# Performance work log

Measured on AMD Instinct MI355X. Metric: run time of the kernel, lower is better.

The kernel has to match this reference:

```python
import jax, jax.numpy as jnp
import numpy as np

R = 40000      # aug_num_rels
E = 500000     # number of relation-graph triplets
DIN = 64       # rel_emb_dim
DH = 64        # hid_dim_rel
H = 8          # num_head
DHID = DH // H # 8
NBIN = 10
L = 2          # num_layer_rel


def _leaky(x):
    return jax.nn.leaky_relu(x, negative_slope=0.2)


def _rel_layer(emb_rel, head, tail, binidx, pw, pb, abin, avec, aw, ab):
    # emb_rel: [R, DH]; head/tail/binidx: [E]
    concat = jnp.concatenate([emb_rel[head], emb_rel[tail]], axis=-1)  # [E, 2*DH]
    z = _leaky(concat @ pw + pb).reshape(-1, H, DHID)                   # [E, H, DHID]
    # attention logits: per-head dot with attn_vec + leaky(bin bias)
    raw = (z * avec[None]).sum(-1) + _leaky(abin[binidx, :, 0])         # [E, H]
    # segmented softmax over edges grouped by head index
    m = jax.ops.segment_max(raw, head, num_segments=R)                  # [R, H]
    e = jnp.exp(raw - m[head])                                          # [E, H]
    s = jax.ops.segment_sum(e, head, num_segments=R)                    # [R, H]
    beta = e / (s[head] + 1e-16)                                        # [E, H]
    msg = (emb_rel[tail] @ aw + ab).reshape(-1, H, DHID) * beta[..., None]
    out = jax.ops.segment_sum(msg, head, num_segments=R)                # [R, H, DHID]
    return out.reshape(R, DH)


def setup_inputs() -> dict:
    key = jax.random.key(0)
    ks = jax.random.split(key, 12)
    ht = jax.random.randint(ks[0], (E, 2), 0, R)
    b = jax.random.randint(ks[1], (E, 1), 0, NBIN)
    relation_triplets = jnp.concatenate([ht, b], axis=-1).astype(jnp.int64)
    sc = 0.05
    return {
        "relation_triplets": relation_triplets,
        "rel_emb_w": jax.random.normal(ks[2], (R, DIN), jnp.float32) * sc,
        "proj1_w": jax.random.normal(ks[3], (DIN, DH), jnp.float32) * sc,
        "proj1_b": jnp.zeros((DH,), jnp.float32),
        "attn_proj_w": jax.random.normal(ks[4], (L, 2 * DH, DH), jnp.float32) * sc,
        "attn_proj_b": jnp.zeros((L, DH), jnp.float32),
        "attn_bin": jax.random.normal(ks[5], (L, NBIN, H, 1), jnp.float32) * sc,
        "attn_vec": jax.random.normal(ks[6], (L, H, DHID), jnp.float32) * sc,
        "aggr_w": jax.random.normal(ks[7], (L, DH, DH), jnp.float32) * sc,
        "aggr_b": jnp.zeros((L, DH), jnp.float32),
        "res_w": jax.random.normal(ks[8], (L, DH, DH), jnp.float32) * sc,
        "res_b": jnp.zeros((L, DH), jnp.float32),
    }


def reference(relation_triplets, rel_emb_w, proj1_w, proj1_b, attn_proj_w,
              attn_proj_b, attn_bin, attn_vec, aggr_w, aggr_b, res_w, res_b):
    head = relation_triplets[:, 0]
    tail = relation_triplets[:, 1]
    binidx = relation_triplets[:, 2]
    emb_rel = jax.nn.relu(rel_emb_w @ proj1_w + proj1_b)  # [R, DH]
    for l in range(L):
        h = _rel_layer(emb_rel, head, tail, binidx,
                       attn_proj_w[l], attn_proj_b[l], attn_bin[l],
                       attn_vec[l], aggr_w[l], aggr_b[l])
        h = jax.nn.relu(h)
        emb_rel = h + jax.nn.relu(emb_rel @ res_w[l] + res_b[l])
    return emb_rel
```

## Files before the change

### kernel.cpp

```cpp
#include <hip/hip_runtime.h>
#include <hip/hip_bf16.h>

typedef __hip_bfloat16 bf16;

#define R_NUM 40000
#define E_NUM 500000
#define HIST_BLOCKS 1954
#define XFA_BLOCKS 1250

#define N_CNTS 0
#define N_ROWP 160000
#define N_STB 320000
#define N_XMP0 2320384
#define N_HR0 12560384
#define N_XMP1 33040384
#define N_HR1 43280384
#define NEED2 63760384ull

#define W_P1W 0
#define W_P1B 4096
#define W_APW 4160
#define W_APB 20544
#define W_ABIN 20672
#define W_AVEC 20832
#define W_AW 20960
#define W_AB 29152
#define W_RW 29280
#define W_RB 37472
#define W_END 37600
#define WCONV_BLOCKS 147

#define O_FLAG 0
#define O_WBUF 256
#define O_ROWP 150784
#define O_CNTS 310784
#define O_TMP 470784
#define O_PART 634624
#define O_STB 635136
#define O_BIG 2635392

static __device__ __forceinline__ float b2f(bf16 x) { return __bfloat162float(x); }
static __device__ __forceinline__ float ldv(const float* p, size_t i) { return p[i]; }
static __device__ __forceinline__ float ldv(const bf16* p, size_t i) { return __bfloat162float(p[i]); }
static __device__ __forceinline__ void stv(float* p, size_t i, float v) { p[i] = v; }
static __device__ __forceinline__ void stv(bf16* p, size_t i, float v) { p[i] = __float2bfloat16(v); }

static __device__ __forceinline__ unsigned int f2bb(float x) {
  union { float f; unsigned int u; } v;
  v.f = x;
  unsigned int r = v.u + 0x7FFFu + ((v.u >> 16) & 1u);
  return r >> 16;
}
static __device__ __forceinline__ unsigned int packxm(float xt, float mt) {
  return f2bb(xt) | (f2bb(mt) << 16);
}

static __device__ __forceinline__ void load_edge(const unsigned int* __restrict__ w, int e,
                                                 int i64, int& h, int& t, int& b) {
  if (i64) {
    h = (int)w[6 * e + 0];
    t = (int)w[6 * e + 2];
    b = (int)w[6 * e + 4];
  } else {
    h = (int)w[3 * e + 0];
    t = (int)w[3 * e + 1];
    b = (int)w[3 * e + 2];
  }
}


__global__ void k_detect_init(const unsigned int* __restrict__ trip_w,
                              const unsigned short* __restrict__ emb_w, int* __restrict__ flag,
                              int* __restrict__ counts, int* __restrict__ stb) {
  int tid = threadIdx.x;
  if (blockIdx.x == 0) {
    if (tid < 64) {
      int lane = tid;
      unsigned int acc = 0;
      for (int i = lane; i < 1024; i += 64) acc |= trip_w[2 * i + 1];
      int votes = 0;
      for (int i = lane; i < 2048; i += 64) {
        unsigned short u = emb_w[2 * i];
        int ex = (u >> 7) & 0xFF;
        if (ex >= 90 && ex <= 130) votes++;
      }
      for (int off = 1; off < 64; off <<= 1) {
        acc |= __shfl_xor(acc, off);
        votes += __shfl_xor(votes, off);
      }
      if (lane == 0) {
        flag[0] = (acc == 0) ? 1 : 0;
        flag[1] = (votes < 1024) ? 1 : 0;
      }
    }
    return;
  }
  int g = (blockIdx.x - 1) * 256 + tid;
  for (int i = g; i < R_NUM; i += 159 * 256) counts[i] = 0;
  if (blockIdx.x == 1 && tid < 64) stb[E_NUM + tid] = 0;
}


template <typename WT, int N>
static __device__ __forceinline__ void xf4t(const float (*sA)[64], int base, int j, int l,
                                            const WT* __restrict__ apw, const WT* __restrict__ apb,
                                            const WT* __restrict__ aw, const WT* __restrict__ ab,
                                            const WT* __restrict__ rw, const WT* __restrict__ rb,
                                            int r0, unsigned int* __restrict__ XMp,
                                            float2* __restrict__ HR) {
  const WT* pwt = apw + l * 8192;
  const WT* pwb = pwt + 4096;
  const WT* awl = aw + l * 4096;
  const WT* rwl = rw + l * 4096;
  float axt[N] = {};
  float amt[N] = {};
  float axh[N] = {};
  float ars[N] = {};
  for (int i4 = 0; i4 < 64; i4 += 4) {
    float4 ev[N];
#pragma unroll
    for (int n = 0; n < N; n++) ev[n] = *(const float4*)&sA[base + n][i4];
#pragma unroll
    for (int di = 0; di < 4; di++) {
      int i = i4 + di;
      float wt = ldv(pwb, (size_t)i * 64 + j);
      float wm = ldv(awl, (size_t)i * 64 + j);
      float wh = ldv(pwt, (size_t)i * 64 + j);
      float wr = ldv(rwl, (size_t)i * 64 + j);
#pragma unroll
      for (int n = 0; n < N; n++) {
        float e = ((const float*)&ev[n])[di];
        axt[n] = fmaf(e, wt, axt[n]);
        amt[n] = fmaf(e, wm, amt[n]);
        axh[n] = fmaf(e, wh, axh[n]);
        ars[n] = fmaf(e, wr, ars[n]);
      }
    }
  }
  float abj = ldv(ab, (size_t)l * 64 + j);
  float pbj = ldv(apb, (size_t)l * 64 + j);
  float rbj = ldv(rb, (size_t)l * 64 + j);
#pragma unroll
  for (int n = 0; n < N; n++) {
    XMp[(size_t)(r0 + n) * 64 + j] = packxm(axt[n], amt[n] + abj);
    HR[(size_t)(r0 + n) * 64 + j] = make_float2(axh[n] + pbj, fmaxf(ars[n] + rbj, 0.f));
  }
}


template <typename T>
static __device__ __forceinline__ void kA_xform(const T* __restrict__ A, const T* __restrict__ p1w,
                                                const T* __restrict__ p1b,
                                                const T* __restrict__ apw,
                                                const T* __restrict__ apb, const T* __restrict__ aw,
                                                const T* __restrict__ ab, const T* __restrict__ rw,
                                                const T* __restrict__ rb, int u,
                                                unsigned int* __restrict__ XMp0,
                                                float2* __restrict__ HR0, float (*sA)[64]) {
  int tid = threadIdx.x;
  int j = tid & 63;
  int g = tid >> 6;
  int base = g * 8;
  for (int k = tid; k < 2048; k += 256) {
    int rr = k >> 6, cc = k & 63;
    sA[rr][cc] = ldv(A, (size_t)(u * 32 + rr) * 64 + cc);
  }
  __syncthreads();
  float a[8] = {0.f, 0.f, 0.f, 0.f, 0.f, 0.f, 0.f, 0.f};
  for (int i4 = 0; i4 < 64; i4 += 4) {
    float4 ev[8];
#pragma unroll
    for (int n = 0; n < 8; n++) ev[n] = *(const float4*)&sA[base + n][i4];
#pragma unroll
    for (int di = 0; di < 4; di++) {
      float wv = ldv(p1w, (size_t)(i4 + di) * 64 + j);
#pragma unroll
      for (int n = 0; n < 8; n++) a[n] = fmaf(((const float*)&ev[n])[di], wv, a[n]);
    }
  }
  float bj = ldv(p1b, j);
#pragma unroll
  for (int n = 0; n < 8; n++) a[n] = fmaxf(a[n] + bj, 0.f);
  __syncthreads();
#pragma unroll
  for (int n = 0; n < 8; n++) sA[base + n][j] = a[n];
  __syncthreads();
  xf4t<T, 8>((const float(*)[64])sA, base, j, 0, apw, apb, aw, ab, rw, rb, u * 32 + base, XMp0,
             HR0);
}

__global__ void __launch_bounds__(256, 4) kA(const unsigned int* __restrict__ trip_w,
                                             const int* __restrict__ flag,
                                             const void* __restrict__ A, const void* p1w,
                                             const void* p1b, const void* apw, const void* apb,
                                             const void* aw, const void* ab, const void* rw,
                                             const void* rb, int* __restrict__ counts,
                                             unsigned int* __restrict__ XMp0,
                                             float2* __restrict__ HR0) {
  if (blockIdx.x >= XFA_BLOCKS) {
    int e = (blockIdx.x - XFA_BLOCKS) * 256 + threadIdx.x;
    if (e < E_NUM) {
      int h = flag[0] ? (int)trip_w[6 * e] : (int)trip_w[3 * e];
      atomicAdd(&counts[h], 1);
    }
    return;
  }
  __shared__ float sA[32][64];
  int u = blockIdx.x;
  if (flag[1])
    kA_xform<float>((const float*)A, (const float*)p1w, (const float*)p1b, (const float*)apw,
                    (const float*)apb, (const float*)aw, (const float*)ab, (const float*)rw,
                    (const float*)rb, u, XMp0, HR0, sA);
  else
    kA_xform<bf16>((const bf16*)A, (const bf16*)p1w, (const bf16*)p1b, (const bf16*)apw,
                   (const bf16*)apb, (const bf16*)aw, (const bf16*)ab, (const bf16*)rw,
                   (const bf16*)rb, u, XMp0, HR0, sA);
}


__global__ void __launch_bounds__(1024) k_scan1(const int* __restrict__ counts,
                                                int* __restrict__ row_ptr) {
  __shared__ int sp[1024];
  int tid = threadIdx.x;
  int base = tid * 40;
  int local[40];
  int s = 0;
  if (base < R_NUM) {
#pragma unroll
    for (int k = 0; k < 40; k++) {
      int v = counts[base + k];
      local[k] = s;
      s += v;
    }
  }
  sp[tid] = s;
  __syncthreads();
  for (int off = 1; off < 1024; off <<= 1) {
    int t = (tid >= off) ? sp[tid - off] : 0;
    __syncthreads();
    sp[tid] += t;
    __syncthreads();
  }
  int pre = (tid == 0) ? 0 : sp[tid - 1];
  if (base < R_NUM) {
#pragma unroll
    for (int k = 0; k < 40; k++) row_ptr[base + k] = pre + local[k];
  }
}

__global__ void k_scatter(const unsigned int* __restrict__ trip_w, const int* __restrict__ flag,
                          int* __restrict__ row_ptr, int* __restrict__ stb) {
  int e = blockIdx.x * 256 + threadIdx.x;
  if (e >= E_NUM) return;
  int h, t, b;
  load_edge(trip_w, e, flag[0], h, t, b);
  int pos = atomicAdd(&row_ptr[h], 1);
  stb[pos] = (t & 0xFFFF) | (b << 16);
}


template <typename T>
static __device__ __forceinline__ void edge_body(int l, const int* __restrict__ row_ptr,
                                                 const int* __restrict__ stb,
                                                 const unsigned int* __restrict__ XMp,
                                                 const float2* __restrict__ HR,
                                                 const T* __restrict__ abin,
                                                 const T* __restrict__ avec,
                                                 float* __restrict__ out, float* sab) {
  int tid = threadIdx.x;
  int lane = tid & 63;
  int w = tid >> 6;
  int hh = lane >> 3;
  if (tid < 80) {
    float a = ldv(abin, (size_t)l * 80 + tid);
    sab[tid] = (a > 0.f) ? a : 0.2f * a;
  }
  __syncthreads();
  float av = ldv(avec, (size_t)l * 64 + lane);

  int r = blockIdx.x * 4 + w;
  float2 hr = HR[(size_t)r * 64 + lane];
  int beg = (r == 0) ? 0 : row_ptr[r - 1];
  int end = row_ptr[r];
  beg = __builtin_amdgcn_readfirstlane(beg);
  end = __builtin_amdgcn_readfirstlane(end);

  float xh = hr.x;
  float num = 0.f, den = 0.f;
  int t0 = (beg < end) ? (stb[beg] & 0xFFFF) : 0;
  for (int jj = beg; jj < end; jj += 16) {
    int pk[16];
    unsigned int xp[16];
#pragma unroll
    for (int k = 0; k < 16; k++) pk[k] = stb[jj + k];
#pragma unroll
    for (int k = 0; k < 16; k++) {
      int t = (jj + k < end) ? (pk[k] & 0xFFFF) : t0;
      xp[k] = XMp[(size_t)t * 64 + lane];
    }
#pragma unroll
    for (int k = 0; k < 16; k++) {
      float xt = __uint_as_float(xp[k] << 16);
      float mt = __uint_as_float(xp[k] & 0xFFFF0000u);
      float z = xh + xt;
      z = (z > 0.f) ? z : 0.2f * z;
      float v = z * av;
      v += __shfl_xor(v, 1);
      v += __shfl_xor(v, 2);
      v += __shfl_xor(v, 4);
      float e = __expf(v + sab[(pk[k] >> 16) * 8 + hh]);
      e = (jj + k < end) ? e : 0.f;
      den += e;
      num = fmaf(mt, e, num);
    }
  }
  out[(size_t)r * 64 + lane] = fmaxf(num / (den + 1e-16f), 0.f) + hr.y;
}

__global__ void __launch_bounds__(256, 8) kE0(const int* __restrict__ row_ptr,
                                              const int* __restrict__ stb,
                                              const int* __restrict__ flag,
                                              const unsigned int* __restrict__ XMp0,
                                              const float2* __restrict__ HR0, const void* abin,
                                              const void* avec, float* __restrict__ emb) {
  __shared__ float sab[80];
  if (flag[1])
    edge_body<float>(0, row_ptr, stb, XMp0, HR0, (const float*)abin, (const float*)avec, emb, sab);
  else
    edge_body<bf16>(0, row_ptr, stb, XMp0, HR0, (const bf16*)abin, (const bf16*)avec, emb, sab);
}

__global__ void __launch_bounds__(256, 8) kC(const int* __restrict__ row_ptr,
                                             const int* __restrict__ stb,
                                             const int* __restrict__ flag,
                                             const unsigned int* __restrict__ XMp1,
                                             const float2* __restrict__ HR1, const void* abin,
                                             const void* avec, float* __restrict__ out) {
  __shared__ float sab[80];
  if (flag[1])
    edge_body<float>(1, row_ptr, stb, XMp1, HR1, (const float*)abin, (const float*)avec, out, sab);
  else
    edge_body<bf16>(1, row_ptr, stb, XMp1, HR1, (const bf16*)abin, (const bf16*)avec, out, sab);
}


template <typename T>
static __device__ __forceinline__ void kX1_body(const float* __restrict__ emb,
                                                const T* __restrict__ apw,
                                                const T* __restrict__ apb, const T* __restrict__ aw,
                                                const T* __restrict__ ab, const T* __restrict__ rw,
                                                const T* __restrict__ rb, int u,
                                                unsigned int* __restrict__ XMp1,
                                                float2* __restrict__ HR1, float (*sE)[64]) {
  int tid = threadIdx.x;
  int j = tid & 63;
  int g = tid >> 6;
  for (int k = tid; k < 2048; k += 256) {
    int rr = k >> 6, cc = k & 63;
    sE[rr][cc] = emb[(size_t)(u * 32 + rr) * 64 + cc];
  }
  __syncthreads();
  xf4t<T, 8>((const float(*)[64])sE, g * 8, j, 1, apw, apb, aw, ab, rw, rb, u * 32 + g * 8, XMp1,
             HR1);
}

__global__ void __launch_bounds__(256, 4) kX1(const float* __restrict__ emb,
                                              const int* __restrict__ flag, const void* apw,
                                              const void* apb, const void* aw, const void* ab,
                                              const void* rw, const void* rb,
                                              unsigned int* __restrict__ XMp1,
                                              float2* __restrict__ HR1) {
  __shared__ float sE[32][64];
  int u = blockIdx.x;
  if (flag[1])
    kX1_body<float>(emb, (const float*)apw, (const float*)apb, (const float*)aw, (const float*)ab,
                    (const float*)rw, (const float*)rb, u, XMp1, HR1, sE);
  else
    kX1_body<bf16>(emb, (const bf16*)apw, (const bf16*)apb, (const bf16*)aw, (const bf16*)ab,
                   (const bf16*)rw, (const bf16*)rb, u, XMp1, HR1, sE);
}


__global__ void k_hist_wconv(const unsigned int* __restrict__ trip_w, const int* __restrict__ flag,
                             int* __restrict__ counts, const void* p1w, const void* p1b,
                             const void* apw, const void* apb, const void* abin, const void* avec,
                             const void* aw, const void* ab, const void* rw, const void* rb,
                             float* __restrict__ wbuf) {
  if (blockIdx.x < WCONV_BLOCKS) {
    int i = blockIdx.x * 256 + threadIdx.x;
    if (i >= W_END) return;
    const void* src;
    int off;
    if (i < W_P1B) { src = p1w; off = i - W_P1W; }
    else if (i < W_APW) { src = p1b; off = i - W_P1B; }
    else if (i < W_APB) { src = apw; off = i - W_APW; }
    else if (i < W_ABIN) { src = apb; off = i - W_APB; }
    else if (i < W_AVEC) { src = abin; off = i - W_ABIN; }
    else if (i < W_AW) { src = avec; off = i - W_AVEC; }
    else if (i < W_AB) { src = aw; off = i - W_AW; }
    else if (i < W_RW) { src = ab; off = i - W_AB; }
    else if (i < W_RB) { src = rw; off = i - W_RW; }
    else { src = rb; off = i - W_RB; }
    wbuf[i] = flag[1] ? ((const float*)src)[off] : b2f(((const bf16*)src)[off]);
    return;
  }
  int e = (blockIdx.x - WCONV_BLOCKS) * 256 + threadIdx.x;
  if (e >= E_NUM) return;
  int h, t, b;
  load_edge(trip_w, e, flag[0], h, t, b);
  atomicAdd(&counts[h], 1);
}

__global__ void k_emb0(const void* __restrict__ A, const int* __restrict__ flag,
                       const float* __restrict__ wbuf, float* __restrict__ emb) {
  int j = threadIdx.x & 63;
  int g = threadIdx.x >> 6;
  int r0 = blockIdx.x * 16 + g * 4;
  int f32 = flag[1];
  __shared__ float sA[16][64];
  for (int k = threadIdx.x; k < 1024; k += 256) {
    int rr = k >> 6, cc = k & 63;
    size_t idx = (size_t)(blockIdx.x * 16 + rr) * 64 + cc;
    sA[rr][cc] = f32 ? ((const float*)A)[idx] : b2f(((const bf16*)A)[idx]);
  }
  __syncthreads();
  const float* W = wbuf + W_P1W;
  float a[4] = {0.f, 0.f, 0.f, 0.f};
  int base = g * 4;
  for (int i = 0; i < 64; i++) {
    float w = W[i * 64 + j];
#pragma unroll
    for (int n = 0; n < 4; n++) a[n] = fmaf(sA[base + n][i], w, a[n]);
  }
  float bj = wbuf[W_P1B + j];
#pragma unroll
  for (int n = 0; n < 4; n++)
    emb[(size_t)(r0 + n) * 64 + j] = fmaxf(a[n] + bj, 0.f);
}

static __device__ __forceinline__ float dotcol(const float* __restrict__ Wm, float val, int lane) {
  float acc = 0.f;
  for (int i = 0; i < 64; i++) acc = fmaf(__shfl(val, i), Wm[i * 64 + lane], acc);
  return acc;
}

template <typename TIN, typename TOUT>
__global__ void k_edge_d(const int* __restrict__ row_ptr, const int* __restrict__ stb,
                         const float* __restrict__ wbuf, int l, const TIN* __restrict__ emb_in,
                         TOUT* __restrict__ emb_out) {
  __shared__ float sab[80];
  int tid = threadIdx.x;
  int lane = tid & 63;
  int w = tid >> 6;
  int r = blockIdx.x * 4 + w;
  int hh = lane >> 3;
  if (tid < 80) {
    float a = wbuf[W_ABIN + l * 80 + tid];
    sab[tid] = (a > 0.f) ? a : 0.2f * a;
  }
  __syncthreads();
  const float* pwt = wbuf + W_APW + l * 8192;
  const float* pwb = pwt + 4096;
  const float* aw = wbuf + W_AW + l * 4096;
  const float* rw = wbuf + W_RW + l * 4096;

  float ev = ldv(emb_in, (size_t)r * 64 + lane);
  float xh = wbuf[W_APB + l * 64 + lane];
  float res = wbuf[W_RB + l * 64 + lane];
  for (int i = 0; i < 64; i++) {
    float e = __shfl(ev, i);
    xh = fmaf(e, pwt[i * 64 + lane], xh);
    res = fmaf(e, rw[i * 64 + lane], res);
  }
  res = fmaxf(res, 0.f);
  float av = wbuf[W_AVEC + l * 64 + lane];
  float abl = wbuf[W_AB + l * 64 + lane];

  int beg = (r == 0) ? 0 : row_ptr[r - 1];
  int end = row_ptr[r];
  float num = 0.f, den = 0.f;
  for (int j = beg; j < end; j++) {
    int p = stb[j];
    int t = p & 0xFFFF;
    float tv = ldv(emb_in, (size_t)t * 64 + lane);
    float z = xh + dotcol(pwb, tv, lane);
    z = (z > 0.f) ? z : 0.2f * z;
    float v = z * av;
    v += __shfl_xor(v, 1);
    v += __shfl_xor(v, 2);
    v += __shfl_xor(v, 4);
    float e = __expf(v + sab[(p >> 16) * 8 + hh]);
    den += e;
    float mt = dotcol(aw, tv, lane) + abl;
    num = fmaf(mt, e, num);
  }
  stv(emb_out, (size_t)r * 64 + lane, fmaxf(num / (den + 1e-16f), 0.f) + res);
}


extern "C" void kernel_launch(void* const* d_in, const int* in_sizes, int n_in,
                              void* d_out, int out_size, void* d_ws, size_t ws_size,
                              hipStream_t stream) {
  const unsigned int* trip_w = (const unsigned int*)d_in[0];
  const void* rel_emb = d_in[1];
  float* emb = (float*)d_out;
  char* ws = (char*)d_ws;

  if (ws_size >= NEED2) {
    int* counts = (int*)(ws + N_CNTS);
    int* row_ptr = (int*)(ws + N_ROWP);
    int* stb = (int*)(ws + N_STB);
    unsigned int* XMp0 = (unsigned int*)(ws + N_XMP0);
    float2* HR0 = (float2*)(ws + N_HR0);
    unsigned int* XMp1 = (unsigned int*)(ws + N_XMP1);
    float2* HR1 = (float2*)(ws + N_HR1);
    int* flag = (int*)(ws + N_STB + (E_NUM + 64) * 4);

    k_detect_init<<<160, 256, 0, stream>>>(trip_w, (const unsigned short*)rel_emb, flag, counts,
                                           stb);
    kA<<<XFA_BLOCKS + HIST_BLOCKS, 256, 0, stream>>>(trip_w, flag, rel_emb, d_in[2], d_in[3],
                                                     d_in[4], d_in[5], d_in[8], d_in[9], d_in[10],
                                                     d_in[11], counts, XMp0, HR0);
    k_scan1<<<1, 1024, 0, stream>>>(counts, row_ptr);
    k_scatter<<<HIST_BLOCKS, 256, 0, stream>>>(trip_w, flag, row_ptr, stb);
    kE0<<<R_NUM / 4, 256, 0, stream>>>(row_ptr, stb, flag, XMp0, HR0, d_in[6], d_in[7], emb);
    kX1<<<XFA_BLOCKS, 256, 0, stream>>>(emb, flag, d_in[4], d_in[5], d_in[8], d_in[9], d_in[10],
                                        d_in[11], XMp1, HR1);
    kC<<<R_NUM / 4, 256, 0, stream>>>(row_ptr, stb, flag, XMp1, HR1, d_in[6], d_in[7], emb);
    return;
  }

  {
    int* flag = (int*)(ws + O_FLAG);
    float* wbuf = (float*)(ws + O_WBUF);
    int* row_ptr = (int*)(ws + O_ROWP);
    int* counts = (int*)(ws + O_CNTS);
    int* stb = (int*)(ws + O_STB);
    char* big = ws + O_BIG;

    k_detect_init<<<160, 256, 0, stream>>>(trip_w, (const unsigned short*)rel_emb, flag, counts,
                                           stb);
    k_hist_wconv<<<WCONV_BLOCKS + HIST_BLOCKS, 256, 0, stream>>>(
        trip_w, flag, counts, d_in[2], d_in[3], d_in[4], d_in[5], d_in[6], d_in[7], d_in[8],
        d_in[9], d_in[10], d_in[11], wbuf);
    k_scan1<<<1, 1024, 0, stream>>>(counts, row_ptr);
    k_scatter<<<HIST_BLOCKS, 256, 0, stream>>>(trip_w, flag, row_ptr, stb);
    k_emb0<<<R_NUM / 16, 256, 0, stream>>>(rel_emb, flag, wbuf, emb);
    bf16* embB = (bf16*)big;
    k_edge_d<float, bf16><<<R_NUM / 4, 256, 0, stream>>>(row_ptr, stb, wbuf, 0, emb, embB);
    k_edge_d<bf16, float><<<R_NUM / 4, 256, 0, stream>>>(row_ptr, stb, wbuf, 1, embB, emb);
  }
}
```

Measured before the change: 258.8 us.

## Record histogram ranks to drop scatter atomics, prefetch weights, grid-stride transforms

The histogram pass now stores each edge's atomicAdd return value as a rank. The scatter then computes its position as row_ptr[h]+rank[e] with no second atomic, and row_ptr becomes an exclusive scan with an extra end entry. The transform kernels also software-prefetch the next four weight rows into registers and run as a fixed grid of 1024 blocks looping over 1250 tiles. This removes contended atomics in the scatter at the cost of an extra 2MB rank buffer, and the prefetching adds register pressure.

Result: slower. 364.5 us (+40.9%).

```diff
diff --git a/kernel.cpp b/kernel.cpp
--- a/kernel.cpp
+++ b/kernel.cpp
@@ -6,16 +6,19 @@
 #define R_NUM 40000
 #define E_NUM 500000
 #define HIST_BLOCKS 1954
-#define XFA_BLOCKS 1250
+#define XF_TILES 1250
+#define XF_GRID 1024
 
 #define N_CNTS 0
 #define N_ROWP 160000
-#define N_STB 320000
-#define N_XMP0 2320384
-#define N_HR0 12560384
-#define N_XMP1 33040384
-#define N_HR1 43280384
-#define NEED2 63760384ull
+#define N_RANK 320256
+#define N_STB 2320384
+#define N_FLAG 4320640
+#define N_XMP0 4320896
+#define N_HR0 14560896
+#define N_XMP1 35040896
+#define N_HR1 45280896
+#define NEED2 65760896ull
 
 #define W_P1W 0
 #define W_P1B 4096
@@ -34,12 +37,12 @@
 #define O_WBUF 256
 #define O_ROWP 150784
 #define O_CNTS 310784
-#define O_TMP 470784
-#define O_PART 634624
 #define O_STB 635136
 #define O_BIG 2635392
 
 static __device__ __forceinline__ float b2f(bf16 x) { return __bfloat162float(x); }
+static __device__ __forceinline__ float cvt(float x) { return x; }
+static __device__ __forceinline__ float cvt(bf16 x) { return __bfloat162float(x); }
 static __device__ __forceinline__ float ldv(const float* p, size_t i) { return p[i]; }
 static __device__ __forceinline__ float ldv(const bf16* p, size_t i) { return __bfloat162float(p[i]); }
 static __device__ __forceinline__ void stv(float* p, size_t i, float v) { p[i] = v; }
@@ -116,17 +119,35 @@
   float amt[N] = {};
   float axh[N] = {};
   float ars[N] = {};
+  WT cw[16];
+#pragma unroll
+  for (int di = 0; di < 4; di++) {
+    size_t o = (size_t)di * 64 + j;
+    cw[di * 4 + 0] = pwb[o];
+    cw[di * 4 + 1] = awl[o];
+    cw[di * 4 + 2] = pwt[o];
+    cw[di * 4 + 3] = rwl[o];
+  }
   for (int i4 = 0; i4 < 64; i4 += 4) {
+    WT nw[16];
+    int i4n = (i4 + 4 < 64) ? i4 + 4 : i4;
+#pragma unroll
+    for (int di = 0; di < 4; di++) {
+      size_t o = (size_t)(i4n + di) * 64 + j;
+      nw[di * 4 + 0] = pwb[o];
+      nw[di * 4 + 1] = awl[o];
+      nw[di * 4 + 2] = pwt[o];
+      nw[di * 4 + 3] = rwl[o];
+    }
     float4 ev[N];
 #pragma unroll
     for (int n = 0; n < N; n++) ev[n] = *(const float4*)&sA[base + n][i4];
 #pragma unroll
     for (int di = 0; di < 4; di++) {
-      int i = i4 + di;
-      float wt = ldv(pwb, (size_t)i * 64 + j);
-      float wm = ldv(awl, (size_t)i * 64 + j);
-      float wh = ldv(pwt, (size_t)i * 64 + j);
-      float wr = ldv(rwl, (size_t)i * 64 + j);
+      float wt = cvt(cw[di * 4 + 0]);
+      float wm = cvt(cw[di * 4 + 1]);
+      float wh = cvt(cw[di * 4 + 2]);
+      float wr = cvt(cw[di * 4 + 3]);
 #pragma unroll
       for (int n = 0; n < N; n++) {
         float e = ((const float*)&ev[n])[di];
@@ -136,6 +157,8 @@
         ars[n] = fmaf(e, wr, ars[n]);
       }
     }
+#pragma unroll
+    for (int k = 0; k < 16; k++) cw[k] = nw[k];
   }
   float abj = ldv(ab, (size_t)l * 64 + j);
   float pbj = ldv(apb, (size_t)l * 64 + j);
@@ -167,16 +190,25 @@
   }
   __syncthreads();
   float a[8] = {0.f, 0.f, 0.f, 0.f, 0.f, 0.f, 0.f, 0.f};
+  T pw[4];
+#pragma unroll
+  for (int di = 0; di < 4; di++) pw[di] = p1w[(size_t)di * 64 + j];
   for (int i4 = 0; i4 < 64; i4 += 4) {
+    T npw[4];
+    int i4n = (i4 + 4 < 64) ? i4 + 4 : i4;
+#pragma unroll
+    for (int di = 0; di < 4; di++) npw[di] = p1w[(size_t)(i4n + di) * 64 + j];
     float4 ev[8];
 #pragma unroll
     for (int n = 0; n < 8; n++) ev[n] = *(const float4*)&sA[base + n][i4];
 #pragma unroll
     for (int di = 0; di < 4; di++) {
-      float wv = ldv(p1w, (size_t)(i4 + di) * 64 + j);
+      float wv = cvt(pw[di]);
 #pragma unroll
       for (int n = 0; n < 8; n++) a[n] = fmaf(((const float*)&ev[n])[di], wv, a[n]);
     }
+#pragma unroll
+    for (int di = 0; di < 4; di++) pw[di] = npw[di];
   }
   float bj = ldv(p1b, j);
 #pragma unroll
@@ -195,26 +227,30 @@
                                              const void* p1b, const void* apw, const void* apb,
                                              const void* aw, const void* ab, const void* rw,
                                              const void* rb, int* __restrict__ counts,
+                                             int* __restrict__ rank,
                                              unsigned int* __restrict__ XMp0,
                                              float2* __restrict__ HR0) {
-  if (blockIdx.x >= XFA_BLOCKS) {
-    int e = (blockIdx.x - XFA_BLOCKS) * 256 + threadIdx.x;
+  if (blockIdx.x >= XF_GRID) {
+    int e = (blockIdx.x - XF_GRID) * 256 + threadIdx.x;
     if (e < E_NUM) {
       int h = flag[0] ? (int)trip_w[6 * e] : (int)trip_w[3 * e];
-      atomicAdd(&counts[h], 1);
+      rank[e] = atomicAdd(&counts[h], 1);
     }
     return;
   }
   __shared__ float sA[32][64];
-  int u = blockIdx.x;
-  if (flag[1])
-    kA_xform<float>((const float*)A, (const float*)p1w, (const float*)p1b, (const float*)apw,
-                    (const float*)apb, (const float*)aw, (const float*)ab, (const float*)rw,
-                    (const float*)rb, u, XMp0, HR0, sA);
-  else
-    kA_xform<bf16>((const bf16*)A, (const bf16*)p1w, (const bf16*)p1b, (const bf16*)apw,
-                   (const bf16*)apb, (const bf16*)aw, (const bf16*)ab, (const bf16*)rw,
-                   (const bf16*)rb, u, XMp0, HR0, sA);
+  int f32 = flag[1];
+  for (int u = blockIdx.x; u < XF_TILES; u += XF_GRID) {
+    if (f32)
+      kA_xform<float>((const float*)A, (const float*)p1w, (const float*)p1b, (const float*)apw,
+                      (const float*)apb, (const float*)aw, (const float*)ab, (const float*)rw,
+                      (const float*)rb, u, XMp0, HR0, sA);
+    else
+      kA_xform<bf16>((const bf16*)A, (const bf16*)p1w, (const bf16*)p1b, (const bf16*)apw,
+                     (const bf16*)apb, (const bf16*)aw, (const bf16*)ab, (const bf16*)rw,
+                     (const bf16*)rb, u, XMp0, HR0, sA);
+    __syncthreads();
+  }
 }
 
 
@@ -246,15 +282,17 @@
 #pragma unroll
     for (int k = 0; k < 40; k++) row_ptr[base + k] = pre + local[k];
   }
-}
-
-__global__ void k_scatter(const unsigned int* __restrict__ trip_w, const int* __restrict__ flag,
-                          int* __restrict__ row_ptr, int* __restrict__ stb) {
+  if (tid == 1023) row_ptr[R_NUM] = sp[1023];
+}
+
+__global__ void k_scatter2(const unsigned int* __restrict__ trip_w, const int* __restrict__ flag,
+                           const int* __restrict__ row_ptr, const int* __restrict__ rank,
+                           int* __restrict__ stb) {
   int e = blockIdx.x * 256 + threadIdx.x;
   if (e >= E_NUM) return;
   int h, t, b;
   load_edge(trip_w, e, flag[0], h, t, b);
-  int pos = atomicAdd(&row_ptr[h], 1);
+  int pos = row_ptr[h] + rank[e];
   stb[pos] = (t & 0xFFFF) | (b << 16);
 }
 
@@ -280,8 +318,8 @@
 
   int r = blockIdx.x * 4 + w;
   float2 hr = HR[(size_t)r * 64 + lane];
-  int beg = (r == 0) ? 0 : row_ptr[r - 1];
-  int end = row_ptr[r];
+  int beg = row_ptr[r];
+  int end = row_ptr[r + 1];
   beg = __builtin_amdgcn_readfirstlane(beg);
   end = __builtin_amdgcn_readfirstlane(end);
 
@@ -371,13 +409,16 @@
                                               unsigned int* __restrict__ XMp1,
                                               float2* __restrict__ HR1) {
   __shared__ float sE[32][64];
-  int u = blockIdx.x;
-  if (flag[1])
-    kX1_body<float>(emb, (const float*)apw, (const float*)apb, (const float*)aw, (const float*)ab,
-                    (const float*)rw, (const float*)rb, u, XMp1, HR1, sE);
-  else
-    kX1_body<bf16>(emb, (const bf16*)apw, (const bf16*)apb, (const bf16*)aw, (const bf16*)ab,
-                   (const bf16*)rw, (const bf16*)rb, u, XMp1, HR1, sE);
+  int f32 = flag[1];
+  for (int u = blockIdx.x; u < XF_TILES; u += XF_GRID) {
+    if (f32)
+      kX1_body<float>(emb, (const float*)apw, (const float*)apb, (const float*)aw,
+                      (const float*)ab, (const float*)rw, (const float*)rb, u, XMp1, HR1, sE);
+    else
+      kX1_body<bf16>(emb, (const bf16*)apw, (const bf16*)apb, (const bf16*)aw, (const bf16*)ab,
+                     (const bf16*)rw, (const bf16*)rb, u, XMp1, HR1, sE);
+    __syncthreads();
+  }
 }
 
 
@@ -411,6 +452,16 @@
   atomicAdd(&counts[h], 1);
 }
 
+__global__ void k_scatter(const unsigned int* __restrict__ trip_w, const int* __restrict__ flag,
+                          int* __restrict__ row_ptr, int* __restrict__ stb) {
+  int e = blockIdx.x * 256 + threadIdx.x;
+  if (e >= E_NUM) return;
+  int h, t, b;
+  load_edge(trip_w, e, flag[0], h, t, b);
+  int pos = atomicAdd(&row_ptr[h], 1);
+  stb[pos] = (t & 0xFFFF) | (b << 16);
+}
+
 __global__ void k_emb0(const void* __restrict__ A, const int* __restrict__ flag,
                        const float* __restrict__ wbuf, float* __restrict__ emb) {
   int j = threadIdx.x & 63;
@@ -509,23 +560,24 @@
   if (ws_size >= NEED2) {
     int* counts = (int*)(ws + N_CNTS);
     int* row_ptr = (int*)(ws + N_ROWP);
+    int* rank = (int*)(ws + N_RANK);
     int* stb = (int*)(ws + N_STB);
+    int* flag = (int*)(ws + N_FLAG);
     unsigned int* XMp0 = (unsigned int*)(ws + N_XMP0);
     float2* HR0 = (float2*)(ws + N_HR0);
     unsigned int* XMp1 = (unsigned int*)(ws + N_XMP1);
     float2* HR1 = (float2*)(ws + N_HR1);
-    int* flag = (int*)(ws + N_STB + (E_NUM + 64) * 4);
 
     k_detect_init<<<160, 256, 0, stream>>>(trip_w, (const unsigned short*)rel_emb, flag, counts,
                                            stb);
-    kA<<<XFA_BLOCKS + HIST_BLOCKS, 256, 0, stream>>>(trip_w, flag, rel_emb, d_in[2], d_in[3],
-                                                     d_in[4], d_in[5], d_in[8], d_in[9], d_in[10],
-                                                     d_in[11], counts, XMp0, HR0);
+    kA<<<XF_GRID + HIST_BLOCKS, 256, 0, stream>>>(trip_w, flag, rel_emb, d_in[2], d_in[3],
+                                                  d_in[4], d_in[5], d_in[8], d_in[9], d_in[10],
+                                                  d_in[11], counts, rank, XMp0, HR0);
     k_scan1<<<1, 1024, 0, stream>>>(counts, row_ptr);
-    k_scatter<<<HIST_BLOCKS, 256, 0, stream>>>(trip_w, flag, row_ptr, stb);
+    k_scatter2<<<HIST_BLOCKS, 256, 0, stream>>>(trip_w, flag, row_ptr, rank, stb);
     kE0<<<R_NUM / 4, 256, 0, stream>>>(row_ptr, stb, flag, XMp0, HR0, d_in[6], d_in[7], emb);
-    kX1<<<XFA_BLOCKS, 256, 0, stream>>>(emb, flag, d_in[4], d_in[5], d_in[8], d_in[9], d_in[10],
-                                        d_in[11], XMp1, HR1);
+    kX1<<<XF_GRID, 256, 0, stream>>>(emb, flag, d_in[4], d_in[5], d_in[8], d_in[9], d_in[10],
+                                     d_in[11], XMp1, HR1);
     kC<<<R_NUM / 4, 256, 0, stream>>>(row_ptr, stb, flag, XMp1, HR1, d_in[6], d_in[7], emb);
     return;
   }
```

## Record per-edge histogram rank and use 64-thread transform blocks

Applied to the files above, without the earlier changes.

The histogram atomic now stores its returned slot into a rank array, so the scatter kernel computes each CSR position as row_ptr[h]+rank[e] without a second atomic. The scan writes an exclusive prefix with a trailing total, and the consumers read beg/end from row_ptr[r] and row_ptr[r+1]. The transform kernels kA and kX1 move from 256-thread blocks of 32 rows to 64-thread blocks of 8 rows, giving four times as many blocks. This removes atomic contention in the scatter and improves spread across CUs, at the cost of an extra 2 MB rank write and read and more weight reloads per row.

Result: faster. 240.4 us (-7.1%).

```diff
diff --git a/kernel.cpp b/kernel.cpp
--- a/kernel.cpp
+++ b/kernel.cpp
@@ -6,16 +6,19 @@
 #define R_NUM 40000
 #define E_NUM 500000
 #define HIST_BLOCKS 1954
-#define XFA_BLOCKS 1250
+#define XF_BLOCKS 5000
+#define HB64 7813
 
 #define N_CNTS 0
 #define N_ROWP 160000
-#define N_STB 320000
-#define N_XMP0 2320384
-#define N_HR0 12560384
-#define N_XMP1 33040384
-#define N_HR1 43280384
-#define NEED2 63760384ull
+#define N_RANK 320256
+#define N_STB 2320384
+#define N_FLAG 4320640
+#define N_XMP0 4320896
+#define N_HR0 14560896
+#define N_XMP1 35040896
+#define N_HR1 45280896
+#define NEED2 65760896ull
 
 #define W_P1W 0
 #define W_P1B 4096
@@ -34,8 +37,6 @@
 #define O_WBUF 256
 #define O_ROWP 150784
 #define O_CNTS 310784
-#define O_TMP 470784
-#define O_PART 634624
 #define O_STB 635136
 #define O_BIG 2635392
 
@@ -101,8 +102,8 @@
 }
 
 
-template <typename WT, int N>
-static __device__ __forceinline__ void xf4t(const float (*sA)[64], int base, int j, int l,
+template <typename WT>
+static __device__ __forceinline__ void xf4t(const float (*sA)[64], int j, int l,
                                             const WT* __restrict__ apw, const WT* __restrict__ apb,
                                             const WT* __restrict__ aw, const WT* __restrict__ ab,
                                             const WT* __restrict__ rw, const WT* __restrict__ rb,
@@ -112,14 +113,14 @@
   const WT* pwb = pwt + 4096;
   const WT* awl = aw + l * 4096;
   const WT* rwl = rw + l * 4096;
-  float axt[N] = {};
-  float amt[N] = {};
-  float axh[N] = {};
-  float ars[N] = {};
+  float axt[8] = {};
+  float amt[8] = {};
+  float axh[8] = {};
+  float ars[8] = {};
   for (int i4 = 0; i4 < 64; i4 += 4) {
-    float4 ev[N];
-#pragma unroll
-    for (int n = 0; n < N; n++) ev[n] = *(const float4*)&sA[base + n][i4];
+    float4 ev[8];
+#pragma unroll
+    for (int n = 0; n < 8; n++) ev[n] = *(const float4*)&sA[n][i4];
 #pragma unroll
     for (int di = 0; di < 4; di++) {
       int i = i4 + di;
@@ -128,7 +129,7 @@
       float wh = ldv(pwt, (size_t)i * 64 + j);
       float wr = ldv(rwl, (size_t)i * 64 + j);
 #pragma unroll
-      for (int n = 0; n < N; n++) {
+      for (int n = 0; n < 8; n++) {
         float e = ((const float*)&ev[n])[di];
         axt[n] = fmaf(e, wt, axt[n]);
         amt[n] = fmaf(e, wm, amt[n]);
@@ -141,7 +142,7 @@
   float pbj = ldv(apb, (size_t)l * 64 + j);
   float rbj = ldv(rb, (size_t)l * 64 + j);
 #pragma unroll
-  for (int n = 0; n < N; n++) {
+  for (int n = 0; n < 8; n++) {
     XMp[(size_t)(r0 + n) * 64 + j] = packxm(axt[n], amt[n] + abj);
     HR[(size_t)(r0 + n) * 64 + j] = make_float2(axh[n] + pbj, fmaxf(ars[n] + rbj, 0.f));
   }
@@ -157,20 +158,18 @@
                                                 const T* __restrict__ rb, int u,
                                                 unsigned int* __restrict__ XMp0,
                                                 float2* __restrict__ HR0, float (*sA)[64]) {
-  int tid = threadIdx.x;
-  int j = tid & 63;
-  int g = tid >> 6;
-  int base = g * 8;
-  for (int k = tid; k < 2048; k += 256) {
+  int j = threadIdx.x;
+  int r0 = u * 8;
+  for (int k = j; k < 512; k += 64) {
     int rr = k >> 6, cc = k & 63;
-    sA[rr][cc] = ldv(A, (size_t)(u * 32 + rr) * 64 + cc);
+    sA[rr][cc] = ldv(A, (size_t)(r0 + rr) * 64 + cc);
   }
   __syncthreads();
   float a[8] = {0.f, 0.f, 0.f, 0.f, 0.f, 0.f, 0.f, 0.f};
   for (int i4 = 0; i4 < 64; i4 += 4) {
     float4 ev[8];
 #pragma unroll
-    for (int n = 0; n < 8; n++) ev[n] = *(const float4*)&sA[base + n][i4];
+    for (int n = 0; n < 8; n++) ev[n] = *(const float4*)&sA[n][i4];
 #pragma unroll
     for (int di = 0; di < 4; di++) {
       float wv = ldv(p1w, (size_t)(i4 + di) * 64 + j);
@@ -183,29 +182,29 @@
   for (int n = 0; n < 8; n++) a[n] = fmaxf(a[n] + bj, 0.f);
   __syncthreads();
 #pragma unroll
-  for (int n = 0; n < 8; n++) sA[base + n][j] = a[n];
-  __syncthreads();
-  xf4t<T, 8>((const float(*)[64])sA, base, j, 0, apw, apb, aw, ab, rw, rb, u * 32 + base, XMp0,
-             HR0);
-}
-
-__global__ void __launch_bounds__(256, 4) kA(const unsigned int* __restrict__ trip_w,
-                                             const int* __restrict__ flag,
-                                             const void* __restrict__ A, const void* p1w,
-                                             const void* p1b, const void* apw, const void* apb,
-                                             const void* aw, const void* ab, const void* rw,
-                                             const void* rb, int* __restrict__ counts,
-                                             unsigned int* __restrict__ XMp0,
-                                             float2* __restrict__ HR0) {
-  if (blockIdx.x >= XFA_BLOCKS) {
-    int e = (blockIdx.x - XFA_BLOCKS) * 256 + threadIdx.x;
+  for (int n = 0; n < 8; n++) sA[n][j] = a[n];
+  __syncthreads();
+  xf4t<T>((const float(*)[64])sA, j, 0, apw, apb, aw, ab, rw, rb, r0, XMp0, HR0);
+}
+
+__global__ void __launch_bounds__(64, 4) kA(const unsigned int* __restrict__ trip_w,
+                                            const int* __restrict__ flag,
+                                            const void* __restrict__ A, const void* p1w,
+                                            const void* p1b, const void* apw, const void* apb,
+                                            const void* aw, const void* ab, const void* rw,
+                                            const void* rb, int* __restrict__ counts,
+                                            int* __restrict__ rank,
+                                            unsigned int* __restrict__ XMp0,
+                                            float2* __restrict__ HR0) {
+  if (blockIdx.x >= XF_BLOCKS) {
+    int e = (blockIdx.x - XF_BLOCKS) * 64 + threadIdx.x;
     if (e < E_NUM) {
       int h = flag[0] ? (int)trip_w[6 * e] : (int)trip_w[3 * e];
-      atomicAdd(&counts[h], 1);
+      rank[e] = atomicAdd(&counts[h], 1);
     }
     return;
   }
-  __shared__ float sA[32][64];
+  __shared__ float sA[8][64];
   int u = blockIdx.x;
   if (flag[1])
     kA_xform<float>((const float*)A, (const float*)p1w, (const float*)p1b, (const float*)apw,
@@ -246,15 +245,17 @@
 #pragma unroll
     for (int k = 0; k < 40; k++) row_ptr[base + k] = pre + local[k];
   }
-}
-
-__global__ void k_scatter(const unsigned int* __restrict__ trip_w, const int* __restrict__ flag,
-                          int* __restrict__ row_ptr, int* __restrict__ stb) {
+  if (tid == 1023) row_ptr[R_NUM] = sp[1023];
+}
+
+__global__ void k_scatter2(const unsigned int* __restrict__ trip_w, const int* __restrict__ flag,
+                           const int* __restrict__ row_ptr, const int* __restrict__ rank,
+                           int* __restrict__ stb) {
   int e = blockIdx.x * 256 + threadIdx.x;
   if (e >= E_NUM) return;
   int h, t, b;
   load_edge(trip_w, e, flag[0], h, t, b);
-  int pos = atomicAdd(&row_ptr[h], 1);
+  int pos = row_ptr[h] + rank[e];
   stb[pos] = (t & 0xFFFF) | (b << 16);
 }
 
@@ -280,8 +281,8 @@
 
   int r = blockIdx.x * 4 + w;
   float2 hr = HR[(size_t)r * 64 + lane];
-  int beg = (r == 0) ? 0 : row_ptr[r - 1];
-  int end = row_ptr[r];
+  int beg = row_ptr[r];
+  int end = row_ptr[r + 1];
   beg = __builtin_amdgcn_readfirstlane(beg);
   end = __builtin_amdgcn_readfirstlane(end);
 
@@ -352,25 +353,22 @@
                                                 const T* __restrict__ rb, int u,
                                                 unsigned int* __restrict__ XMp1,
                                                 float2* __restrict__ HR1, float (*sE)[64]) {
-  int tid = threadIdx.x;
-  int j = tid & 63;
-  int g = tid >> 6;
-  for (int k = tid; k < 2048; k += 256) {
+  int j = threadIdx.x;
+  for (int k = j; k < 512; k += 64) {
     int rr = k >> 6, cc = k & 63;
-    sE[rr][cc] = emb[(size_t)(u * 32 + rr) * 64 + cc];
-  }
-  __syncthreads();
-  xf4t<T, 8>((const float(*)[64])sE, g * 8, j, 1, apw, apb, aw, ab, rw, rb, u * 32 + g * 8, XMp1,
-             HR1);
-}
-
-__global__ void __launch_bounds__(256, 4) kX1(const float* __restrict__ emb,
-                                              const int* __restrict__ flag, const void* apw,
-                                              const void* apb, const void* aw, const void* ab,
-                                              const void* rw, const void* rb,
-                                              unsigned int* __restrict__ XMp1,
-                                              float2* __restrict__ HR1) {
-  __shared__ float sE[32][64];
+    sE[rr][cc] = emb[(size_t)(u * 8 + rr) * 64 + cc];
+  }
+  __syncthreads();
+  xf4t<T>((const float(*)[64])sE, j, 1, apw, apb, aw, ab, rw, rb, u * 8, XMp1, HR1);
+}
+
+__global__ void __launch_bounds__(64, 4) kX1(const float* __restrict__ emb,
+                                             const int* __restrict__ flag, const void* apw,
+                                             const void* apb, const void* aw, const void* ab,
+                                             const void* rw, const void* rb,
+                                             unsigned int* __restrict__ XMp1,
+                                             float2* __restrict__ HR1) {
+  __shared__ float sE[8][64];
   int u = blockIdx.x;
   if (flag[1])
     kX1_body<float>(emb, (const float*)apw, (const float*)apb, (const float*)aw, (const float*)ab,
@@ -411,6 +409,16 @@
   atomicAdd(&counts[h], 1);
 }
 
+__global__ void k_scatter(const unsigned int* __restrict__ trip_w, const int* __restrict__ flag,
+                          int* __restrict__ row_ptr, int* __restrict__ stb) {
+  int e = blockIdx.x * 256 + threadIdx.x;
+  if (e >= E_NUM) return;
+  int h, t, b;
+  load_edge(trip_w, e, flag[0], h, t, b);
+  int pos = atomicAdd(&row_ptr[h], 1);
+  stb[pos] = (t & 0xFFFF) | (b << 16);
+}
+
 __global__ void k_emb0(const void* __restrict__ A, const int* __restrict__ flag,
                        const float* __restrict__ wbuf, float* __restrict__ emb) {
   int j = threadIdx.x & 63;
@@ -509,23 +517,24 @@
   if (ws_size >= NEED2) {
     int* counts = (int*)(ws + N_CNTS);
     int* row_ptr = (int*)(ws + N_ROWP);
+    int* rank = (int*)(ws + N_RANK);
     int* stb = (int*)(ws + N_STB);
+    int* flag = (int*)(ws + N_FLAG);
     unsigned int* XMp0 = (unsigned int*)(ws + N_XMP0);
     float2* HR0 = (float2*)(ws + N_HR0);
     unsigned int* XMp1 = (unsigned int*)(ws + N_XMP1);
     float2* HR1 = (float2*)(ws + N_HR1);
-    int* flag = (int*)(ws + N_STB + (E_NUM + 64) * 4);
 
     k_detect_init<<<160, 256, 0, stream>>>(trip_w, (const unsigned short*)rel_emb, flag, counts,
                                            stb);
-    kA<<<XFA_BLOCKS + HIST_BLOCKS, 256, 0, stream>>>(trip_w, flag, rel_emb, d_in[2], d_in[3],
-                                                     d_in[4], d_in[5], d_in[8], d_in[9], d_in[10],
-                                                     d_in[11], counts, XMp0, HR0);
+    kA<<<XF_BLOCKS + HB64, 64, 0, stream>>>(trip_w, flag, rel_emb, d_in[2], d_in[3], d_in[4],
+                                            d_in[5], d_in[8], d_in[9], d_in[10], d_in[11],
+                                            counts, rank, XMp0, HR0);
     k_scan1<<<1, 1024, 0, stream>>>(counts, row_ptr);
-    k_scatter<<<HIST_BLOCKS, 256, 0, stream>>>(trip_w, flag, row_ptr, stb);
+    k_scatter2<<<HIST_BLOCKS, 256, 0, stream>>>(trip_w, flag, row_ptr, rank, stb);
     kE0<<<R_NUM / 4, 256, 0, stream>>>(row_ptr, stb, flag, XMp0, HR0, d_in[6], d_in[7], emb);
-    kX1<<<XFA_BLOCKS, 256, 0, stream>>>(emb, flag, d_in[4], d_in[5], d_in[8], d_in[9], d_in[10],
-                                        d_in[11], XMp1, HR1);
+    kX1<<<XF_BLOCKS, 64, 0, stream>>>(emb, flag, d_in[4], d_in[5], d_in[8], d_in[9], d_in[10],
+                                      d_in[11], XMp1, HR1);
     kC<<<R_NUM / 4, 256, 0, stream>>>(row_ptr, stb, flag, XMp1, HR1, d_in[6], d_in[7], emb);
     return;
   }
```
